# Performance work log

Measured on AMD Instinct MI355X. Metric: run time of the kernel, lower is better.

Reference implementation:

```python
import jax, jax.numpy as jnp
import numpy as np

B, N, D = 8, 256, 128   # batch, nodes, feature width
MID, OUT = 128, 128
FEAT = 2 * D            # concat(n_features, hidden)


def _glorot(key, fan_in, fan_out):
    s = (2.0 / (fan_in + fan_out)) ** 0.5
    return jax.random.normal(key, (fan_in, fan_out), dtype=jnp.float32) * s


def setup_inputs() -> dict:
    key = jax.random.key(0)
    ks = jax.random.split(key, 12)
    inp = {
        "hidden": jax.random.normal(ks[0], (B, N, D), dtype=jnp.float32),
        "n_features": jax.random.normal(ks[1], (B, N, D), dtype=jnp.float32),
        "e_features": jax.random.normal(ks[2], (B, N, N, D), dtype=jnp.float32),
        "g_features": jax.random.normal(ks[3], (B, D), dtype=jnp.float32),
        "adj": jax.random.bernoulli(ks[4], 0.5, (B, N, N)).astype(jnp.float32),
        # Linear params (haiku Linear: y = x @ w + b)
        "W1": _glorot(ks[5], FEAT, MID), "b1": jnp.zeros((MID,), jnp.float32),
        "W2": _glorot(ks[6], FEAT, MID), "b2": jnp.zeros((MID,), jnp.float32),
        "We": _glorot(ks[7], D, MID),    "be": jnp.zeros((MID,), jnp.float32),
        "Wg": _glorot(ks[8], D, MID),    "bg": jnp.zeros((MID,), jnp.float32),
        "Wo1": _glorot(ks[9], FEAT, OUT), "bo1": jnp.zeros((OUT,), jnp.float32),
        "Wo2": _glorot(ks[10], MID, OUT), "bo2": jnp.zeros((OUT,), jnp.float32),
    }
    return inp


def reference(hidden, n_features, e_features, g_features, adj,
              W1, b1, W2, b2, We, be, Wg, bg, Wo1, bo1, Wo2, bo2):
    # features: (B, N, 2D)
    features = jnp.concatenate([n_features, hidden], axis=-1)
    msg_1 = features @ W1 + b1              # (B, N, MID)
    msg_2 = features @ W2 + b2              # (B, N, MID)
    msg_e = e_features @ We + be            # (B, N, N, MID)
    msg_g = g_features @ Wg + bg            # (B, MID)
    # broadcast-add: msgs[b, i, j] = msg_1[b, j] + msg_2[b, i] + msg_e[b, i, j] + msg_g[b]
    msgs = (msg_1[:, None, :, :] + msg_2[:, :, None, :]
            + msg_e + msg_g[:, None, None, :])  # (B, N, N, MID)
    # masked max reduction over axis=1 (default reduction=jnp.max branch)
    msgs = jnp.max(msgs * adj[..., None], axis=1)  # (B, N, MID)
    ret = (features @ Wo1 + bo1) + (msgs @ Wo2 + bo2)  # (B, N, OUT)
    return ret
```

## Files before the change

kernel.cpp:

```cpp
#include <hip/hip_runtime.h>
#include <stdint.h>

#define B_   8
#define N_   256
#define D_   128
#define MID_ 128
#define FEAT_ 256

typedef __attribute__((ext_vector_type(4))) float  floatx4;
typedef __attribute__((ext_vector_type(8))) __bf16 bf16x8;

__device__ __forceinline__ floatx4 mfma16(bf16x8 a, bf16x8 b, floatx4 c) {
    return __builtin_amdgcn_mfma_f32_16x16x32_bf16(a, b, c, 0, 0, 0);
}

__device__ __forceinline__ bf16x8 cvt8(floatx4 a, floatx4 b) {
    bf16x8 r;
    r[0] = (__bf16)a[0]; r[1] = (__bf16)a[1]; r[2] = (__bf16)a[2]; r[3] = (__bf16)a[3];
    r[4] = (__bf16)b[0]; r[5] = (__bf16)b[1]; r[6] = (__bf16)b[2]; r[7] = (__bf16)b[3];
    return r;
}

__global__ void kG(const float* __restrict__ g, const float* __restrict__ Wg,
                   const float* __restrict__ bg, const float* __restrict__ b1,
                   const float* __restrict__ be, float* __restrict__ gplus) {
    int t = threadIdx.x;
    int b = t >> 7, m = t & 127;
    float acc = 0.f;
    for (int k = 0; k < D_; ++k)
        acc += g[b * D_ + k] * Wg[k * MID_ + m];
    gplus[b * MID_ + m] = acc + bg[m] + b1[m] + be[m];
}

__global__ void __launch_bounds__(256)
kA(const float* __restrict__ nfeat, const float* __restrict__ hidden,
   const float* __restrict__ W1, const float* __restrict__ W2,
   const float* __restrict__ Wo1, const float* __restrict__ gplus,
   const float* __restrict__ b2, const float* __restrict__ bo1,
   const float* __restrict__ bo2,
   float* __restrict__ C, float* __restrict__ msg2, float* __restrict__ retA) {
    __shared__ __bf16 Wb[8 * 8 * 64 * 8];
    int t = threadIdx.x;
    int wid = blockIdx.y;
    const float* W = (wid == 0) ? W1 : ((wid == 1) ? W2 : Wo1);
    for (int idx = t; idx < 32768; idx += 256) {
        int k = idx >> 7, m = idx & 127;
        Wb[(((k >> 5) * 8 + (m >> 4)) * 64 + ((k >> 3) & 3) * 16 + (m & 15)) * 8 + (k & 7)]
            = (__bf16)W[idx];
    }
    __syncthreads();

    int lane = t & 63, w = t >> 6;
    int n16 = lane & 15, quad = lane >> 4;
    int R = blockIdx.x * 64 + w * 16 + n16;
    int b = R >> 8;
    const float* frow0 = nfeat  + (size_t)R * D_ + quad * 8;
    const float* frow1 = hidden + (size_t)R * D_ + quad * 8;

    bf16x8 bfrag[8];
#pragma unroll
    for (int ks = 0; ks < 8; ++ks) {
        const float* p = (ks < 4) ? (frow0 + ks * 32) : (frow1 + (ks - 4) * 32);
        floatx4 v0 = *(const floatx4*)p;
        floatx4 v1 = *(const floatx4*)(p + 4);
        bfrag[ks] = cvt8(v0, v1);
    }

    float* outp = (wid == 0) ? C : ((wid == 1) ? msg2 : retA);
#pragma unroll 2
    for (int mt = 0; mt < 8; ++mt) {
        floatx4 acc = (floatx4)0.f;
#pragma unroll
        for (int ks = 0; ks < 8; ++ks) {
            bf16x8 a = *(const bf16x8*)&Wb[((ks * 8 + mt) * 64 + lane) * 8];
            acc = mfma16(a, bfrag[ks], acc);
        }
        int m0 = mt * 16 + quad * 4;
        floatx4 add;
        if (wid == 0)      add = *(const floatx4*)&gplus[b * MID_ + m0];
        else if (wid == 1) add = *(const floatx4*)&b2[m0];
        else {
            floatx4 x = *(const floatx4*)&bo1[m0];
            floatx4 y = *(const floatx4*)&bo2[m0];
            add = x + y;
        }
        *(floatx4*)&outp[(size_t)R * MID_ + m0] = acc + add;
    }
}

__global__ void __launch_bounds__(256, 4)
kB(const float* __restrict__ e, const float* __restrict__ We,
   const float* __restrict__ adj, const float* __restrict__ C,
   const float* __restrict__ msg2, const float* __restrict__ retA,
   const float* __restrict__ Wo2, float* __restrict__ out) {
    __shared__ __bf16 Wb[4 * 8 * 64 * 8];
    __shared__ float adj_sh[N_];
    __shared__ float C_sh[MID_];
    __shared__ float wmax[4][MID_];
    __shared__ float msgs_sh[MID_];
    __shared__ float part[2][MID_];

    int t = threadIdx.x;
    int b = blockIdx.x >> 8, j = blockIdx.x & 255;

    for (int idx = t; idx < 16384; idx += 256) {
        int k = idx >> 7, m = idx & 127;
        Wb[(((k >> 5) * 8 + (m >> 4)) * 64 + ((k >> 3) & 3) * 16 + (m & 15)) * 8 + (k & 7)]
            = (__bf16)We[idx];
    }
    adj_sh[t] = adj[b * N_ * N_ + t * N_ + j];
    if (t < 128) C_sh[t] = C[(b * N_ + j) * MID_ + t];
    __syncthreads();

    int lane = t & 63, w = t >> 6;
    int n16 = lane & 15, quad = lane >> 4;
    const float* ebase = e + (size_t)b * N_ * N_ * D_ + (size_t)j * D_ + quad * 8;
    const float* m2b   = msg2 + (size_t)b * N_ * MID_;

    floatx4 rm[8];
#pragma unroll
    for (int mt = 0; mt < 8; ++mt) rm[mt] = (floatx4)(-INFINITY);

    for (int pass = 0; pass < 2; ++pass) {
        int ibase = pass * 128 + w * 32;
        bf16x8 ef[2][4];
#pragma unroll
        for (int it = 0; it < 2; ++it) {
            const float* rowp = ebase + (size_t)(ibase + it * 16 + n16) * (N_ * D_);
#pragma unroll
            for (int ks = 0; ks < 4; ++ks) {
                floatx4 v0 = *(const floatx4*)(rowp + ks * 32);
                floatx4 v1 = *(const floatx4*)(rowp + ks * 32 + 4);
                ef[it][ks] = cvt8(v0, v1);
            }
        }
        float adj0 = adj_sh[ibase + n16];
        float adj1 = adj_sh[ibase + 16 + n16];
        const float* m2r0 = m2b + (size_t)(ibase + n16) * MID_;
        const float* m2r1 = m2b + (size_t)(ibase + 16 + n16) * MID_;

#pragma unroll 2
        for (int mt = 0; mt < 8; ++mt) {
            floatx4 a0 = (floatx4)0.f, a1 = (floatx4)0.f;
#pragma unroll
            for (int ks = 0; ks < 4; ++ks) {
                bf16x8 aW = *(const bf16x8*)&Wb[((ks * 8 + mt) * 64 + lane) * 8];
                a0 = mfma16(aW, ef[0][ks], a0);
                a1 = mfma16(aW, ef[1][ks], a1);
            }
            int m0 = mt * 16 + quad * 4;
            floatx4 c4  = *(const floatx4*)&C_sh[m0];
            floatx4 m20 = *(const floatx4*)&m2r0[m0];
            floatx4 m21 = *(const floatx4*)&m2r1[m0];
#pragma unroll
            for (int r = 0; r < 4; ++r) {
                float v0 = (a0[r] + c4[r] + m20[r]) * adj0;
                float v1 = (a1[r] + c4[r] + m21[r]) * adj1;
                rm[mt][r] = fmaxf(rm[mt][r], fmaxf(v0, v1));
            }
        }
    }

#pragma unroll
    for (int mt = 0; mt < 8; ++mt) {
#pragma unroll
        for (int r = 0; r < 4; ++r) {
            float v = rm[mt][r];
            v = fmaxf(v, __shfl_xor(v, 1, 64));
            v = fmaxf(v, __shfl_xor(v, 2, 64));
            v = fmaxf(v, __shfl_xor(v, 4, 64));
            v = fmaxf(v, __shfl_xor(v, 8, 64));
            rm[mt][r] = v;
        }
    }
    if (n16 == 0) {
#pragma unroll
        for (int mt = 0; mt < 8; ++mt)
            *(floatx4*)&wmax[w][mt * 16 + quad * 4] = rm[mt];
    }
    __syncthreads();

    int m = t & 127, h = t >> 7;
    if (t < 128) {
        float mx = fmaxf(fmaxf(wmax[0][m], wmax[1][m]), fmaxf(wmax[2][m], wmax[3][m]));
        msgs_sh[m] = mx;
    }
    __syncthreads();

    float a2 = 0.f;
    for (int k = h * 64; k < h * 64 + 64; ++k)
        a2 += msgs_sh[k] * Wo2[k * MID_ + m];
    part[h][m] = a2;
    __syncthreads();
    if (t < 128) {
        int R = b * N_ + j;
        out[(size_t)R * MID_ + m] = retA[R * MID_ + m] + part[0][m] + part[1][m];
    }
}

extern "C" void kernel_launch(void* const* d_in, const int* in_sizes, int n_in,
                              void* d_out, int out_size, void* d_ws, size_t ws_size,
                              hipStream_t stream) {
    (void)in_sizes; (void)n_in; (void)out_size; (void)ws_size;
    const float* hidden = (const float*)d_in[0];
    const float* nfeat  = (const float*)d_in[1];
    const float* e      = (const float*)d_in[2];
    const float* g      = (const float*)d_in[3];
    const float* adj    = (const float*)d_in[4];
    const float* W1  = (const float*)d_in[5];
    const float* b1  = (const float*)d_in[6];
    const float* W2  = (const float*)d_in[7];
    const float* b2  = (const float*)d_in[8];
    const float* We  = (const float*)d_in[9];
    const float* be  = (const float*)d_in[10];
    const float* Wg  = (const float*)d_in[11];
    const float* bg  = (const float*)d_in[12];
    const float* Wo1 = (const float*)d_in[13];
    const float* bo1 = (const float*)d_in[14];
    const float* Wo2 = (const float*)d_in[15];
    const float* bo2 = (const float*)d_in[16];
    float* outp = (float*)d_out;

    float* ws    = (float*)d_ws;
    float* gplus = ws;
    float* C     = ws + 1024;
    float* msg2  = C + 262144;
    float* retA  = msg2 + 262144;

    kG<<<1, 1024, 0, stream>>>(g, Wg, bg, b1, be, gplus);
    kA<<<dim3(32, 3), 256, 0, stream>>>(nfeat, hidden, W1, W2, Wo1, gplus,
                                        b2, bo1, bo2, C, msg2, retA);
    kB<<<2048, 256, 0, stream>>>(e, We, adj, C, msg2, retA, Wo2, outp);
}
```

Before: 446.4 us.

## Fuse global-feature GEMV into kA, vectorize weight staging, software-pipeline edge loads in kB

Drops the separate single-block kG launch and computes the per-batch global term inside kA's wid==0 blocks, keeping it in shared memory. Weight staging into LDS now reads float4 rows and writes packed bf16 pairs instead of scalar stores. kB's edge-feature loop is restructured to process one 16-row tile at a time while prefetching the next tile's raw fp32 data into registers, with msg2 rows preloaded. Two M-tiles share each edge fragment. Launch bounds for kB are relaxed to 3 waves per SIMD to fit the extra registers, which may reduce occupancy.

```diff
diff --git a/kernel.cpp b/kernel.cpp
--- a/kernel.cpp
+++ b/kernel.cpp
@@ -21,39 +21,54 @@
     return r;
 }
 
-__global__ void kG(const float* __restrict__ g, const float* __restrict__ Wg,
-                   const float* __restrict__ bg, const float* __restrict__ b1,
-                   const float* __restrict__ be, float* __restrict__ gplus) {
-    int t = threadIdx.x;
-    int b = t >> 7, m = t & 127;
-    float acc = 0.f;
-    for (int k = 0; k < D_; ++k)
-        acc += g[b * D_ + k] * Wg[k * MID_ + m];
-    gplus[b * MID_ + m] = acc + bg[m] + b1[m] + be[m];
+__device__ __forceinline__ unsigned int pack2(float lo, float hi) {
+    unsigned short u0 = __builtin_bit_cast(unsigned short, (__bf16)lo);
+    unsigned short u1 = __builtin_bit_cast(unsigned short, (__bf16)hi);
+    return (unsigned int)u0 | ((unsigned int)u1 << 16);
+}
+
+__device__ __forceinline__ int widx(int k, int m) {
+    return ((((k >> 5) * 8 + (m >> 4)) * 64 + ((k >> 3) & 3) * 16 + (m & 15)) << 3) + (k & 7);
 }
 
 __global__ void __launch_bounds__(256)
 kA(const float* __restrict__ nfeat, const float* __restrict__ hidden,
    const float* __restrict__ W1, const float* __restrict__ W2,
-   const float* __restrict__ Wo1, const float* __restrict__ gplus,
+   const float* __restrict__ Wo1,
+   const float* __restrict__ g, const float* __restrict__ Wg,
+   const float* __restrict__ bg, const float* __restrict__ b1,
+   const float* __restrict__ be,
    const float* __restrict__ b2, const float* __restrict__ bo1,
    const float* __restrict__ bo2,
    float* __restrict__ C, float* __restrict__ msg2, float* __restrict__ retA) {
-    __shared__ __bf16 Wb[8 * 8 * 64 * 8];
+    __shared__ unsigned short Wb[8 * 8 * 64 * 8];
+    __shared__ float gplus_sh[MID_];
     int t = threadIdx.x;
     int wid = blockIdx.y;
+    int bidx = blockIdx.x >> 2;
     const float* W = (wid == 0) ? W1 : ((wid == 1) ? W2 : Wo1);
-    for (int idx = t; idx < 32768; idx += 256) {
-        int k = idx >> 7, m = idx & 127;
-        Wb[(((k >> 5) * 8 + (m >> 4)) * 64 + ((k >> 3) & 3) * 16 + (m & 15)) * 8 + (k & 7)]
-            = (__bf16)W[idx];
+#pragma unroll
+    for (int it = 0; it < 16; ++it) {
+        int id = t + it * 256;
+        int m0 = (id & 31) * 4;
+        int k0 = (id >> 5) * 2;
+        floatx4 a = *(const floatx4*)&W[k0 * MID_ + m0];
+        floatx4 bb = *(const floatx4*)&W[(k0 + 1) * MID_ + m0];
+#pragma unroll
+        for (int p = 0; p < 4; ++p)
+            *(unsigned int*)&Wb[widx(k0, m0 + p)] = pack2(a[p], bb[p]);
+    }
+    if (wid == 0 && t < 128) {
+        float acc = 0.f;
+        for (int k = 0; k < D_; ++k)
+            acc += g[bidx * D_ + k] * Wg[k * MID_ + t];
+        gplus_sh[t] = acc + bg[t] + b1[t] + be[t];
     }
     __syncthreads();
 
     int lane = t & 63, w = t >> 6;
     int n16 = lane & 15, quad = lane >> 4;
     int R = blockIdx.x * 64 + w * 16 + n16;
-    int b = R >> 8;
     const float* frow0 = nfeat  + (size_t)R * D_ + quad * 8;
     const float* frow1 = hidden + (size_t)R * D_ + quad * 8;
 
@@ -72,12 +87,12 @@
         floatx4 acc = (floatx4)0.f;
 #pragma unroll
         for (int ks = 0; ks < 8; ++ks) {
-            bf16x8 a = *(const bf16x8*)&Wb[((ks * 8 + mt) * 64 + lane) * 8];
+            bf16x8 a = *(const bf16x8*)&Wb[((ks * 8 + mt) * 64 + lane) << 3];
             acc = mfma16(a, bfrag[ks], acc);
         }
         int m0 = mt * 16 + quad * 4;
         floatx4 add;
-        if (wid == 0)      add = *(const floatx4*)&gplus[b * MID_ + m0];
+        if (wid == 0)      add = *(const floatx4*)&gplus_sh[m0];
         else if (wid == 1) add = *(const floatx4*)&b2[m0];
         else {
             floatx4 x = *(const floatx4*)&bo1[m0];
@@ -88,12 +103,12 @@
     }
 }
 
-__global__ void __launch_bounds__(256, 4)
+__global__ void __launch_bounds__(256, 3)
 kB(const float* __restrict__ e, const float* __restrict__ We,
    const float* __restrict__ adj, const float* __restrict__ C,
    const float* __restrict__ msg2, const float* __restrict__ retA,
    const float* __restrict__ Wo2, float* __restrict__ out) {
-    __shared__ __bf16 Wb[4 * 8 * 64 * 8];
+    __shared__ unsigned short Wb[4 * 8 * 64 * 8];
     __shared__ float adj_sh[N_];
     __shared__ float C_sh[MID_];
     __shared__ float wmax[4][MID_];
@@ -103,10 +118,16 @@
     int t = threadIdx.x;
     int b = blockIdx.x >> 8, j = blockIdx.x & 255;
 
-    for (int idx = t; idx < 16384; idx += 256) {
-        int k = idx >> 7, m = idx & 127;
-        Wb[(((k >> 5) * 8 + (m >> 4)) * 64 + ((k >> 3) & 3) * 16 + (m & 15)) * 8 + (k & 7)]
-            = (__bf16)We[idx];
+#pragma unroll
+    for (int it = 0; it < 8; ++it) {
+        int id = t + it * 256;
+        int m0 = (id & 31) * 4;
+        int k0 = (id >> 5) * 2;
+        floatx4 a = *(const floatx4*)&We[k0 * MID_ + m0];
+        floatx4 bb = *(const floatx4*)&We[(k0 + 1) * MID_ + m0];
+#pragma unroll
+        for (int p = 0; p < 4; ++p)
+            *(unsigned int*)&Wb[widx(k0, m0 + p)] = pack2(a[p], bb[p]);
     }
     adj_sh[t] = adj[b * N_ * N_ + t * N_ + j];
     if (t < 128) C_sh[t] = C[(b * N_ + j) * MID_ + t];
@@ -121,42 +142,59 @@
 #pragma unroll
     for (int mt = 0; mt < 8; ++mt) rm[mt] = (floatx4)(-INFINITY);
 
-    for (int pass = 0; pass < 2; ++pass) {
-        int ibase = pass * 128 + w * 32;
-        bf16x8 ef[2][4];
-#pragma unroll
-        for (int it = 0; it < 2; ++it) {
-            const float* rowp = ebase + (size_t)(ibase + it * 16 + n16) * (N_ * D_);
+    floatx4 raw[8];
+    floatx4 m2v[8];
+    bf16x8  ef[4];
+
+    {
+        const float* rp = ebase + (size_t)(w * 64 + n16) * (N_ * D_);
+#pragma unroll
+        for (int ks = 0; ks < 4; ++ks) {
+            raw[2 * ks]     = *(const floatx4*)(rp + ks * 32);
+            raw[2 * ks + 1] = *(const floatx4*)(rp + ks * 32 + 4);
+        }
+    }
+
+#pragma unroll
+    for (int t_ = 0; t_ < 4; ++t_) {
+        int i = w * 64 + t_ * 16 + n16;
+#pragma unroll
+        for (int ks = 0; ks < 4; ++ks) ef[ks] = cvt8(raw[2 * ks], raw[2 * ks + 1]);
+        if (t_ < 3) {
+            const float* rp = ebase + (size_t)(i + 16) * (N_ * D_);
 #pragma unroll
             for (int ks = 0; ks < 4; ++ks) {
-                floatx4 v0 = *(const floatx4*)(rowp + ks * 32);
-                floatx4 v1 = *(const floatx4*)(rowp + ks * 32 + 4);
-                ef[it][ks] = cvt8(v0, v1);
+                raw[2 * ks]     = *(const floatx4*)(rp + ks * 32);
+                raw[2 * ks + 1] = *(const floatx4*)(rp + ks * 32 + 4);
             }
         }
-        float adj0 = adj_sh[ibase + n16];
-        float adj1 = adj_sh[ibase + 16 + n16];
-        const float* m2r0 = m2b + (size_t)(ibase + n16) * MID_;
-        const float* m2r1 = m2b + (size_t)(ibase + 16 + n16) * MID_;
-
-#pragma unroll 2
-        for (int mt = 0; mt < 8; ++mt) {
+        {
+            const float* mp = m2b + (size_t)i * MID_;
+#pragma unroll
+            for (int mt = 0; mt < 8; ++mt)
+                m2v[mt] = *(const floatx4*)&mp[mt * 16 + quad * 4];
+        }
+        float adjc = adj_sh[i];
+
+#pragma unroll
+        for (int mtp = 0; mtp < 4; ++mtp) {
             floatx4 a0 = (floatx4)0.f, a1 = (floatx4)0.f;
 #pragma unroll
             for (int ks = 0; ks < 4; ++ks) {
-                bf16x8 aW = *(const bf16x8*)&Wb[((ks * 8 + mt) * 64 + lane) * 8];
-                a0 = mfma16(aW, ef[0][ks], a0);
-                a1 = mfma16(aW, ef[1][ks], a1);
+                bf16x8 aW0 = *(const bf16x8*)&Wb[((ks * 8 + 2 * mtp) * 64 + lane) << 3];
+                bf16x8 aW1 = *(const bf16x8*)&Wb[((ks * 8 + 2 * mtp + 1) * 64 + lane) << 3];
+                a0 = mfma16(aW0, ef[ks], a0);
+                a1 = mfma16(aW1, ef[ks], a1);
             }
-            int m0 = mt * 16 + quad * 4;
-            floatx4 c4  = *(const floatx4*)&C_sh[m0];
-            floatx4 m20 = *(const floatx4*)&m2r0[m0];
-            floatx4 m21 = *(const floatx4*)&m2r1[m0];
+            int m0 = (2 * mtp) * 16 + quad * 4;
+            floatx4 c0 = *(const floatx4*)&C_sh[m0];
+            floatx4 c1 = *(const floatx4*)&C_sh[m0 + 16];
 #pragma unroll
             for (int r = 0; r < 4; ++r) {
-                float v0 = (a0[r] + c4[r] + m20[r]) * adj0;
-                float v1 = (a1[r] + c4[r] + m21[r]) * adj1;
-                rm[mt][r] = fmaxf(rm[mt][r], fmaxf(v0, v1));
+                float v0 = (a0[r] + c0[r] + m2v[2 * mtp][r]) * adjc;
+                float v1 = (a1[r] + c1[r] + m2v[2 * mtp + 1][r]) * adjc;
+                rm[2 * mtp][r]     = fmaxf(rm[2 * mtp][r], v0);
+                rm[2 * mtp + 1][r] = fmaxf(rm[2 * mtp + 1][r], v1);
             }
         }
     }
@@ -221,14 +259,13 @@
     const float* bo2 = (const float*)d_in[16];
     float* outp = (float*)d_out;
 
-    float* ws    = (float*)d_ws;
-    float* gplus = ws;
-    float* C     = ws + 1024;
-    float* msg2  = C + 262144;
-    float* retA  = msg2 + 262144;
-
-    kG<<<1, 1024, 0, stream>>>(g, Wg, bg, b1, be, gplus);
-    kA<<<dim3(32, 3), 256, 0, stream>>>(nfeat, hidden, W1, W2, Wo1, gplus,
-                                        b2, bo1, bo2, C, msg2, retA);
+    float* ws   = (float*)d_ws;
+    float* C    = ws;
+    float* msg2 = C + 262144;
+    float* retA = msg2 + 262144;
+
+    kA<<<dim3(32, 3), 256, 0, stream>>>(nfeat, hidden, W1, W2, Wo1,
+                                        g, Wg, bg, b1, be, b2, bo1, bo2,
+                                        C, msg2, retA);
     kB<<<2048, 256, 0, stream>>>(e, We, adj, C, msg2, retA, Wo2, outp);
 }
```

New measurement: 540.8 us. +21.2%, slower.
